# Optimization experiments

Measured on AMD Instinct MI355X. Metric: run time of the kernel, lower is better.

Reference implementation:

```python
import jax, jax.numpy as jnp
import numpy as np

N_NODES = 50000
N_EDGES = 500000
D_MODEL = 256
N_HEADS = 8
D_K = D_MODEL // N_HEADS


def setup_inputs() -> dict:
    key = jax.random.key(0)
    ks = jax.random.split(key, 12)
    s = 1.0 / np.sqrt(D_MODEL)
    inp = {
        "query": jax.random.normal(ks[0], (N_NODES, D_MODEL), dtype=jnp.float32),
        "key": jax.random.normal(ks[1], (N_NODES, D_MODEL), dtype=jnp.float32),
        "value": jax.random.normal(ks[2], (N_NODES, D_MODEL), dtype=jnp.float32),
        "edges": jax.random.randint(ks[3], (2, N_EDGES), 0, N_NODES, dtype=jnp.int64),
        # four nn.Linear(d_model, d_model) layers: q, k, v, out
        "Wq": jax.random.uniform(ks[4], (D_MODEL, D_MODEL), jnp.float32, -s, s),
        "bq": jax.random.uniform(ks[5], (D_MODEL,), jnp.float32, -s, s),
        "Wk": jax.random.uniform(ks[6], (D_MODEL, D_MODEL), jnp.float32, -s, s),
        "bk": jax.random.uniform(ks[7], (D_MODEL,), jnp.float32, -s, s),
        "Wv": jax.random.uniform(ks[8], (D_MODEL, D_MODEL), jnp.float32, -s, s),
        "bv": jax.random.uniform(ks[9], (D_MODEL,), jnp.float32, -s, s),
        "Wo": jax.random.uniform(ks[10], (D_MODEL, D_MODEL), jnp.float32, -s, s),
        "bo": jax.random.uniform(ks[11], (D_MODEL,), jnp.float32, -s, s),
    }
    return inp


def reference(query, key, value, edges, Wq, bq, Wk, bk, Wv, bv, Wo, bo):
    N = query.shape[0]
    # linear projections (torch Linear: x @ W.T + b), view as [N, h, d_k]
    q = (query @ Wq.T + bq).reshape(N, N_HEADS, D_K)
    k = (key @ Wk.T + bk).reshape(N, N_HEADS, D_K)
    v = (value @ Wv.T + bv).reshape(N, N_HEADS, D_K)

    dst, src = edges[0], edges[1]
    # per-edge dot-product scores [E, h]
    scores = jnp.einsum("ehd,ehd->eh", q[dst], k[src]) / jnp.sqrt(
        jnp.asarray(D_K, dtype=q.dtype)
    )
    # segment softmax over destination node neighborhoods (per head)
    m = jax.ops.segment_max(scores, dst, num_segments=N)  # [N, h]
    ex = jnp.exp(scores - m[dst])
    den = jax.ops.segment_sum(ex, dst, num_segments=N)  # [N, h]
    p_attn = ex / den[dst]  # [E, h]

    # weighted scatter-sum of gathered values -> [N, h, d_k]
    out = jax.ops.segment_sum(p_attn[:, :, None] * v[src], dst, num_segments=N)
    out = out.reshape(N, D_MODEL)
    return out @ Wo.T + bo
```

## Files before the change

### kernel.cpp

```cpp
#include <hip/hip_runtime.h>
#include <hip/hip_bf16.h>
#include <cstdint>

#define D_MODEL 256
#define NHEADS 8
#define DK 32
#define LDSPAD 4
#define LDSROW (D_MODEL + LDSPAD)
#define BM 64

typedef float f32x4 __attribute__((ext_vector_type(4)));
typedef __bf16 bf16x8 __attribute__((ext_vector_type(8)));

__device__ __forceinline__ unsigned short f2bf_rne(float f) {
    unsigned int u = __float_as_uint(f);
    u += 0x7FFF + ((u >> 16) & 1);
    return (unsigned short)(u >> 16);
}
__device__ __forceinline__ float bf2f(unsigned short h) {
    return __uint_as_float(((unsigned int)h) << 16);
}

__global__ void conv_weights_hist(const float* __restrict__ W0, const float* __restrict__ W1,
                                  const float* __restrict__ W2, const float* __restrict__ W3,
                                  unsigned short* __restrict__ out,
                                  const int* __restrict__ dst, int E,
                                  int* __restrict__ counts) {
    int i = blockIdx.x * blockDim.x + threadIdx.x;
    if (i < 4 * 8192) {
        const int w    = i >> 13;
        const int rem  = i & 8191;
        const int lane = rem & 63;
        const int kk   = (rem >> 6) & 7;
        const int ntile= rem >> 9;
        const int row  = ntile * 16 + (lane & 15);
        const int col  = kk * 32 + (lane >> 4) * 8;
        const float* Wsrc = (w == 0) ? W0 : (w == 1) ? W1 : (w == 2) ? W2 : W3;
        const float* sp = Wsrc + (size_t)row * D_MODEL + col;
        float4 x0 = *(const float4*)sp;
        float4 x1 = *(const float4*)(sp + 4);
        unsigned short* dp = out + (size_t)w * D_MODEL * D_MODEL + (size_t)rem * 8;
        ushort4 o0, o1;
        o0.x = f2bf_rne(x0.x); o0.y = f2bf_rne(x0.y); o0.z = f2bf_rne(x0.z); o0.w = f2bf_rne(x0.w);
        o1.x = f2bf_rne(x1.x); o1.y = f2bf_rne(x1.y); o1.z = f2bf_rne(x1.z); o1.w = f2bf_rne(x1.w);
        *(ushort4*)dp = o0;
        *(ushort4*)(dp + 4) = o1;
    } else {
        const int e = i - 4 * 8192;
        if (e < E) atomicAdd(&counts[dst[e]], 1);
    }
}

__global__ __launch_bounds__(512, 4) void gemm_qkv(
    const float* __restrict__ Aq, const float* __restrict__ Ak, const float* __restrict__ Av,
    const unsigned short* __restrict__ Wsw,
    const float* __restrict__ bq, const float* __restrict__ bk, const float* __restrict__ bv,
    unsigned short* __restrict__ qbuf, unsigned short* __restrict__ kvbuf,
    int M)
{
    __shared__ __align__(16) unsigned short smem[BM * LDSROW];

    const int which = blockIdx.y;
    const float* A = (which == 0) ? Aq : (which == 1) ? Ak : Av;
    const float* bias = (which == 0) ? bq : (which == 1) ? bk : bv;
    const unsigned short* Wb = Wsw + (size_t)which * D_MODEL * D_MODEL;
    unsigned short* outp = (which == 0) ? qbuf : kvbuf;
    const int out_stride = (which == 0) ? D_MODEL : 2 * D_MODEL;
    const int out_off    = (which == 2) ? D_MODEL : 0;

    const int lane  = threadIdx.x & 63;
    const int wave  = threadIdx.x >> 6;
    const int mrow  = lane & 15;
    const int quad  = lane >> 4;
    const int m0    = blockIdx.x * BM;

    bf16x8 bfr[2][8];
#pragma unroll
    for (int ni = 0; ni < 2; ++ni)
#pragma unroll
        for (int kk = 0; kk < 8; ++kk)
            bfr[ni][kk] = *(const bf16x8*)(Wb + ((size_t)((wave * 2 + ni) * 8 + kk) * 64 + lane) * 8);

    float bcol[2];
#pragma unroll
    for (int ni = 0; ni < 2; ++ni) bcol[ni] = bias[wave * 32 + ni * 16 + mrow];

#pragma unroll
    for (int half = 0; half < 2; ++half) {
        float4 x[4];
#pragma unroll
        for (int i = 0; i < 4; ++i) {
            const int g = (half * 4 + i) * 512 + threadIdx.x;
            const int r = g >> 6, c4 = g & 63;
            const int grow = min(m0 + r, M - 1);
            x[i] = *(const float4*)(A + (size_t)grow * D_MODEL + c4 * 4);
        }
#pragma unroll
        for (int i = 0; i < 4; ++i) {
            const int g = (half * 4 + i) * 512 + threadIdx.x;
            const int r = g >> 6, c4 = g & 63;
            ushort4 o;
            o.x = f2bf_rne(x[i].x); o.y = f2bf_rne(x[i].y);
            o.z = f2bf_rne(x[i].z); o.w = f2bf_rne(x[i].w);
            *(ushort4*)(smem + r * LDSROW + c4 * 4) = o;
        }
    }
    __syncthreads();

    f32x4 acc[4][2] = {};
#pragma unroll
    for (int kk = 0; kk < 8; ++kk) {
        bf16x8 afr[4];
#pragma unroll
        for (int mi = 0; mi < 4; ++mi)
            afr[mi] = *(const bf16x8*)(smem + (mi * 16 + mrow) * LDSROW + kk * 32 + quad * 8);
#pragma unroll
        for (int mi = 0; mi < 4; ++mi)
#pragma unroll
            for (int ni = 0; ni < 2; ++ni)
                acc[mi][ni] = __builtin_amdgcn_mfma_f32_16x16x32_bf16(
                    afr[mi], bfr[ni][kk], acc[mi][ni], 0, 0, 0);
    }

#pragma unroll
    for (int mi = 0; mi < 4; ++mi)
#pragma unroll
        for (int r = 0; r < 4; ++r) {
            const int row = m0 + mi * 16 + quad * 4 + r;
            if (row < M) {
#pragma unroll
                for (int ni = 0; ni < 2; ++ni)
                    outp[(size_t)row * out_stride + out_off + wave * 32 + ni * 16 + mrow] =
                        f2bf_rne(acc[mi][ni][r] + bcol[ni]);
            }
        }
}

__global__ __launch_bounds__(512, 4) void gemm_out(
    const unsigned short* __restrict__ Ab, const unsigned short* __restrict__ Wb,
    const float* __restrict__ bias, float* __restrict__ outp, int M)
{
    __shared__ __align__(16) unsigned short smem[BM * LDSROW];

    const int lane  = threadIdx.x & 63;
    const int wave  = threadIdx.x >> 6;
    const int mrow  = lane & 15;
    const int quad  = lane >> 4;
    const int m0    = blockIdx.x * BM;

    bf16x8 bfr[2][8];
#pragma unroll
    for (int ni = 0; ni < 2; ++ni)
#pragma unroll
        for (int kk = 0; kk < 8; ++kk)
            bfr[ni][kk] = *(const bf16x8*)(Wb + ((size_t)((wave * 2 + ni) * 8 + kk) * 64 + lane) * 8);

    float bcol[2];
#pragma unroll
    for (int ni = 0; ni < 2; ++ni) bcol[ni] = bias[wave * 32 + ni * 16 + mrow];

#pragma unroll
    for (int i = 0; i < 4; ++i) {
        const int g = i * 512 + threadIdx.x;
        const int r = g >> 5, c8 = g & 31;
        const int grow = min(m0 + r, M - 1);
        bf16x8 x = *(const bf16x8*)(Ab + (size_t)grow * D_MODEL + c8 * 8);
        *(bf16x8*)(smem + r * LDSROW + c8 * 8) = x;
    }
    __syncthreads();

    f32x4 acc[4][2] = {};
#pragma unroll
    for (int kk = 0; kk < 8; ++kk) {
        bf16x8 afr[4];
#pragma unroll
        for (int mi = 0; mi < 4; ++mi)
            afr[mi] = *(const bf16x8*)(smem + (mi * 16 + mrow) * LDSROW + kk * 32 + quad * 8);
#pragma unroll
        for (int mi = 0; mi < 4; ++mi)
#pragma unroll
            for (int ni = 0; ni < 2; ++ni)
                acc[mi][ni] = __builtin_amdgcn_mfma_f32_16x16x32_bf16(
                    afr[mi], bfr[ni][kk], acc[mi][ni], 0, 0, 0);
    }

#pragma unroll
    for (int mi = 0; mi < 4; ++mi)
#pragma unroll
        for (int r = 0; r < 4; ++r) {
            const int row = m0 + mi * 16 + quad * 4 + r;
            if (row < M) {
#pragma unroll
                for (int ni = 0; ni < 2; ++ni)
                    outp[(size_t)row * D_MODEL + wave * 32 + ni * 16 + mrow] =
                        acc[mi][ni][r] + bcol[ni];
            }
        }
}

__global__ void block_reduce_kernel(const int* __restrict__ counts, int N,
                                    int* __restrict__ blockSums) {
    const int g = blockIdx.x * 256 + threadIdx.x;
    int v = (g < N) ? counts[g] : 0;
#pragma unroll
    for (int d = 1; d < 64; d <<= 1) v += __shfl_xor(v, d);
    __shared__ int ws[4];
    if ((threadIdx.x & 63) == 0) ws[threadIdx.x >> 6] = v;
    __syncthreads();
    if (threadIdx.x == 0) blockSums[blockIdx.x] = ws[0] + ws[1] + ws[2] + ws[3];
}

__global__ void scan_blocks_kernel(int* __restrict__ blockSums, int G) {
    __shared__ int sh[256];
    const int t = threadIdx.x;
    int v = (t < G) ? blockSums[t] : 0;
    sh[t] = v;
    __syncthreads();
#pragma unroll
    for (int off = 1; off < 256; off <<= 1) {
        int add = (t >= off) ? sh[t - off] : 0;
        __syncthreads();
        sh[t] += add;
        __syncthreads();
    }
    if (t < G) blockSums[t] = sh[t] - v;
}

__global__ void scan_write_kernel(const int* __restrict__ counts, int N,
                                  const int* __restrict__ blockOffsets,
                                  int* __restrict__ offsets) {
    const int g = blockIdx.x * 256 + threadIdx.x;
    const int t = threadIdx.x;
    int v = (g < N) ? counts[g] : 0;
    __shared__ int sh[256];
    sh[t] = v;
    __syncthreads();
#pragma unroll
    for (int off = 1; off < 256; off <<= 1) {
        int add = (t >= off) ? sh[t - off] : 0;
        __syncthreads();
        sh[t] += add;
        __syncthreads();
    }
    if (g <= N) offsets[g] = sh[t] - v + blockOffsets[blockIdx.x];
}

__global__ void fill_kernel(const int* __restrict__ dst, const int* __restrict__ src, int E,
                            const int* __restrict__ offsets, int* __restrict__ cursor,
                            int* __restrict__ ssrc) {
    int i = blockIdx.x * blockDim.x + threadIdx.x;
    if (i < E) {
        int d = dst[i];
        int r = atomicAdd(&cursor[d], 1);
        ssrc[offsets[d] + r] = src[i];
    }
}

__global__ __launch_bounds__(256) void attn_kernel(
    const unsigned short* __restrict__ qb, const unsigned short* __restrict__ kv,
    const int* __restrict__ offsets, const int* __restrict__ ssrc,
    unsigned short* __restrict__ attn, int N)
{
    const int node = blockIdx.x * 4 + (threadIdx.x >> 6);
    if (node >= N) return;
    const int lane = threadIdx.x & 63;

    ushort4 qu = *(const ushort4*)(qb + (size_t)node * D_MODEL + 4 * lane);
    const float sc = 0.17677669529663689f;
    float qx = bf2f(qu.x) * sc, qy = bf2f(qu.y) * sc,
          qz = bf2f(qu.z) * sc, qw = bf2f(qu.w) * sc;

    float m = -INFINITY, l = 0.f;
    float ax = 0.f, ay = 0.f, az = 0.f, aw = 0.f;

    const int e0 = offsets[node], e1 = offsets[node + 1];
    int e = e0;

    for (; e + 7 < e1; e += 8) {
        const unsigned short* b0 = kv + (size_t)ssrc[e]     * 512 + 4 * lane;
        const unsigned short* b1 = kv + (size_t)ssrc[e + 1] * 512 + 4 * lane;
        const unsigned short* b2 = kv + (size_t)ssrc[e + 2] * 512 + 4 * lane;
        const unsigned short* b3 = kv + (size_t)ssrc[e + 3] * 512 + 4 * lane;
        const unsigned short* b4 = kv + (size_t)ssrc[e + 4] * 512 + 4 * lane;
        const unsigned short* b5 = kv + (size_t)ssrc[e + 5] * 512 + 4 * lane;
        const unsigned short* b6 = kv + (size_t)ssrc[e + 6] * 512 + 4 * lane;
        const unsigned short* b7 = kv + (size_t)ssrc[e + 7] * 512 + 4 * lane;
        ushort4 k0 = *(const ushort4*)b0, v0 = *(const ushort4*)(b0 + D_MODEL);
        ushort4 k1 = *(const ushort4*)b1, v1 = *(const ushort4*)(b1 + D_MODEL);
        ushort4 k2 = *(const ushort4*)b2, v2 = *(const ushort4*)(b2 + D_MODEL);
        ushort4 k3 = *(const ushort4*)b3, v3 = *(const ushort4*)(b3 + D_MODEL);
        ushort4 k4 = *(const ushort4*)b4, v4 = *(const ushort4*)(b4 + D_MODEL);
        ushort4 k5 = *(const ushort4*)b5, v5 = *(const ushort4*)(b5 + D_MODEL);
        ushort4 k6 = *(const ushort4*)b6, v6 = *(const ushort4*)(b6 + D_MODEL);
        ushort4 k7 = *(const ushort4*)b7, v7 = *(const ushort4*)(b7 + D_MODEL);

        float p0 = qx * bf2f(k0.x) + qy * bf2f(k0.y) + qz * bf2f(k0.z) + qw * bf2f(k0.w);
        float p1 = qx * bf2f(k1.x) + qy * bf2f(k1.y) + qz * bf2f(k1.z) + qw * bf2f(k1.w);
        float p2 = qx * bf2f(k2.x) + qy * bf2f(k2.y) + qz * bf2f(k2.z) + qw * bf2f(k2.w);
        float p3 = qx * bf2f(k3.x) + qy * bf2f(k3.y) + qz * bf2f(k3.z) + qw * bf2f(k3.w);
        float p4 = qx * bf2f(k4.x) + qy * bf2f(k4.y) + qz * bf2f(k4.z) + qw * bf2f(k4.w);
        float p5 = qx * bf2f(k5.x) + qy * bf2f(k5.y) + qz * bf2f(k5.z) + qw * bf2f(k5.w);
        float p6 = qx * bf2f(k6.x) + qy * bf2f(k6.y) + qz * bf2f(k6.z) + qw * bf2f(k6.w);
        float p7 = qx * bf2f(k7.x) + qy * bf2f(k7.y) + qz * bf2f(k7.z) + qw * bf2f(k7.w);
#pragma unroll
        for (int d = 1; d <= 4; d <<= 1) {
            p0 += __shfl_xor(p0, d); p1 += __shfl_xor(p1, d);
            p2 += __shfl_xor(p2, d); p3 += __shfl_xor(p3, d);
            p4 += __shfl_xor(p4, d); p5 += __shfl_xor(p5, d);
            p6 += __shfl_xor(p6, d); p7 += __shfl_xor(p7, d);
        }
        float mnew = fmaxf(fmaxf(fmaxf(fmaxf(m, p0), fmaxf(p1, p2)), fmaxf(fmaxf(p3, p4), fmaxf(p5, p6))), p7);
        float alpha = __expf(m - mnew);
        float w0 = __expf(p0 - mnew), w1 = __expf(p1 - mnew);
        float w2 = __expf(p2 - mnew), w3 = __expf(p3 - mnew);
        float w4 = __expf(p4 - mnew), w5 = __expf(p5 - mnew);
        float w6 = __expf(p6 - mnew), w7 = __expf(p7 - mnew);
        ax = ax * alpha + w0 * bf2f(v0.x) + w1 * bf2f(v1.x) + w2 * bf2f(v2.x) + w3 * bf2f(v3.x)
                        + w4 * bf2f(v4.x) + w5 * bf2f(v5.x) + w6 * bf2f(v6.x) + w7 * bf2f(v7.x);
        ay = ay * alpha + w0 * bf2f(v0.y) + w1 * bf2f(v1.y) + w2 * bf2f(v2.y) + w3 * bf2f(v3.y)
                        + w4 * bf2f(v4.y) + w5 * bf2f(v5.y) + w6 * bf2f(v6.y) + w7 * bf2f(v7.y);
        az = az * alpha + w0 * bf2f(v0.z) + w1 * bf2f(v1.z) + w2 * bf2f(v2.z) + w3 * bf2f(v3.z)
                        + w4 * bf2f(v4.z) + w5 * bf2f(v5.z) + w6 * bf2f(v6.z) + w7 * bf2f(v7.z);
        aw = aw * alpha + w0 * bf2f(v0.w) + w1 * bf2f(v1.w) + w2 * bf2f(v2.w) + w3 * bf2f(v3.w)
                        + w4 * bf2f(v4.w) + w5 * bf2f(v5.w) + w6 * bf2f(v6.w) + w7 * bf2f(v7.w);
        l = l * alpha + w0 + w1 + w2 + w3 + w4 + w5 + w6 + w7;
        m = mnew;
    }

    for (; e + 3 < e1; e += 4) {
        const unsigned short* b0 = kv + (size_t)ssrc[e]     * 512 + 4 * lane;
        const unsigned short* b1 = kv + (size_t)ssrc[e + 1] * 512 + 4 * lane;
        const unsigned short* b2 = kv + (size_t)ssrc[e + 2] * 512 + 4 * lane;
        const unsigned short* b3 = kv + (size_t)ssrc[e + 3] * 512 + 4 * lane;
        ushort4 k0 = *(const ushort4*)b0, v0 = *(const ushort4*)(b0 + D_MODEL);
        ushort4 k1 = *(const ushort4*)b1, v1 = *(const ushort4*)(b1 + D_MODEL);
        ushort4 k2 = *(const ushort4*)b2, v2 = *(const ushort4*)(b2 + D_MODEL);
        ushort4 k3 = *(const ushort4*)b3, v3 = *(const ushort4*)(b3 + D_MODEL);

        float p0 = qx * bf2f(k0.x) + qy * bf2f(k0.y) + qz * bf2f(k0.z) + qw * bf2f(k0.w);
        float p1 = qx * bf2f(k1.x) + qy * bf2f(k1.y) + qz * bf2f(k1.z) + qw * bf2f(k1.w);
        float p2 = qx * bf2f(k2.x) + qy * bf2f(k2.y) + qz * bf2f(k2.z) + qw * bf2f(k2.w);
        float p3 = qx * bf2f(k3.x) + qy * bf2f(k3.y) + qz * bf2f(k3.z) + qw * bf2f(k3.w);
#pragma unroll
        for (int d = 1; d <= 4; d <<= 1) {
            p0 += __shfl_xor(p0, d); p1 += __shfl_xor(p1, d);
            p2 += __shfl_xor(p2, d); p3 += __shfl_xor(p3, d);
        }
        float mnew = fmaxf(fmaxf(fmaxf(m, p0), fmaxf(p1, p2)), p3);
        float alpha = __expf(m - mnew);
        float w0 = __expf(p0 - mnew), w1 = __expf(p1 - mnew);
        float w2 = __expf(p2 - mnew), w3 = __expf(p3 - mnew);
        ax = ax * alpha + w0 * bf2f(v0.x) + w1 * bf2f(v1.x) + w2 * bf2f(v2.x) + w3 * bf2f(v3.x);
        ay = ay * alpha + w0 * bf2f(v0.y) + w1 * bf2f(v1.y) + w2 * bf2f(v2.y) + w3 * bf2f(v3.y);
        az = az * alpha + w0 * bf2f(v0.z) + w1 * bf2f(v1.z) + w2 * bf2f(v2.z) + w3 * bf2f(v3.z);
        aw = aw * alpha + w0 * bf2f(v0.w) + w1 * bf2f(v1.w) + w2 * bf2f(v2.w) + w3 * bf2f(v3.w);
        l = l * alpha + w0 + w1 + w2 + w3;
        m = mnew;
    }

    for (; e < e1; ++e) {
        const unsigned short* b = kv + (size_t)ssrc[e] * 512 + 4 * lane;
        ushort4 ku = *(const ushort4*)b;
        ushort4 vu = *(const ushort4*)(b + D_MODEL);
        float p = qx * bf2f(ku.x) + qy * bf2f(ku.y) + qz * bf2f(ku.z) + qw * bf2f(ku.w);
        p += __shfl_xor(p, 1);
        p += __shfl_xor(p, 2);
        p += __shfl_xor(p, 4);
        float mnew  = fmaxf(m, p);
        float alpha = __expf(m - mnew);
        float w     = __expf(p - mnew);
        ax = ax * alpha + w * bf2f(vu.x);
        ay = ay * alpha + w * bf2f(vu.y);
        az = az * alpha + w * bf2f(vu.z);
        aw = aw * alpha + w * bf2f(vu.w);
        l = l * alpha + w;
        m = mnew;
    }

    const float inv = (l > 0.f) ? 1.f / l : 0.f;
    ushort4 o;
    o.x = f2bf_rne(ax * inv);
    o.y = f2bf_rne(ay * inv);
    o.z = f2bf_rne(az * inv);
    o.w = f2bf_rne(aw * inv);
    *(ushort4*)(attn + (size_t)node * D_MODEL + 4 * lane) = o;
}

extern "C" void kernel_launch(void* const* d_in, const int* in_sizes, int n_in,
                              void* d_out, int out_size, void* d_ws, size_t ws_size,
                              hipStream_t stream)
{
    const float* query = (const float*)d_in[0];
    const float* key   = (const float*)d_in[1];
    const float* value = (const float*)d_in[2];
    const int*   edges = (const int*)d_in[3];
    const float* Wq = (const float*)d_in[4];
    const float* bq = (const float*)d_in[5];
    const float* Wk = (const float*)d_in[6];
    const float* bk = (const float*)d_in[7];
    const float* Wv = (const float*)d_in[8];
    const float* bv = (const float*)d_in[9];
    const float* Wo = (const float*)d_in[10];
    const float* bo = (const float*)d_in[11];
    float* out = (float*)d_out;

    const int N = in_sizes[0] / D_MODEL;
    const int E = in_sizes[3] / 2;
    const int* dst = edges;
    const int* src = edges + E;

    char* ws = (char*)d_ws;
    size_t off = 0;
    auto alloc = [&](size_t bytes) {
        void* p = ws + off;
        off += (bytes + 255) & ~(size_t)255;
        return p;
    };
    unsigned short* qbuf  = (unsigned short*)alloc((size_t)N * D_MODEL * 2);
    unsigned short* kvbuf = (unsigned short*)alloc((size_t)N * 2 * D_MODEL * 2);
    unsigned short* attnb = (unsigned short*)alloc((size_t)N * D_MODEL * 2);
    unsigned short* Wbuf  = (unsigned short*)alloc((size_t)4 * D_MODEL * D_MODEL * 2);
    int*            counts  = (int*)alloc((size_t)2 * N * 4);
    int*            offsets = (int*)alloc((size_t)(N + 1) * 4);
    int*            ssrc    = (int*)alloc((size_t)E * 4);
    int*            bsums   = (int*)alloc((size_t)256 * 4);

    hipMemsetAsync(counts, 0, (size_t)2 * N * 4, stream);

    const int fused_threads = 4 * 8192 + E;
    conv_weights_hist<<<(fused_threads + 255) / 256, 256, 0, stream>>>(
        Wq, Wk, Wv, Wo, Wbuf, dst, E, counts);

    const int mtiles = (N + BM - 1) / BM;
    gemm_qkv<<<dim3(mtiles, 3), 512, 0, stream>>>(query, key, value, Wbuf,
                                                  bq, bk, bv, qbuf, kvbuf, N);

    const int G = (N + 256) / 256;
    block_reduce_kernel<<<G, 256, 0, stream>>>(counts, N, bsums);
    scan_blocks_kernel<<<1, 256, 0, stream>>>(bsums, G);
    scan_write_kernel<<<G, 256, 0, stream>>>(counts, N, bsums, offsets);

    const int eblocks = (E + 255) / 256;
    fill_kernel<<<eblocks, 256, 0, stream>>>(dst, src, E, offsets, counts + N, ssrc);
    attn_kernel<<<(N + 3) / 4, 256, 0, stream>>>(qbuf, kvbuf, offsets, ssrc, attnb, N);

    gemm_out<<<mtiles, 512, 0, stream>>>(attnb, Wbuf + 3 * D_MODEL * D_MODEL, bo, out, N);
}
```

Before: 371.5 us.

## Make projection GEMMs persistent with register-prefetched double-buffered LDS tiles

```diff
diff --git a/kernel.cpp b/kernel.cpp
--- a/kernel.cpp
+++ b/kernel.cpp
@@ -7,7 +7,9 @@
 #define DK 32
 #define LDSPAD 4
 #define LDSROW (D_MODEL + LDSPAD)
-#define BM 64
+#define QBM 32
+#define QBLK 171
+#define OBLK 512
 
 typedef float f32x4 __attribute__((ext_vector_type(4)));
 typedef __bf16 bf16x8 __attribute__((ext_vector_type(8)));
@@ -56,9 +58,9 @@
     const unsigned short* __restrict__ Wsw,
     const float* __restrict__ bq, const float* __restrict__ bk, const float* __restrict__ bv,
     unsigned short* __restrict__ qbuf, unsigned short* __restrict__ kvbuf,
-    int M)
+    int M, int mtiles)
 {
-    __shared__ __align__(16) unsigned short smem[BM * LDSROW];
+    __shared__ __align__(16) unsigned short smem[2 * QBM * LDSROW];
 
     const int which = blockIdx.y;
     const float* A = (which == 0) ? Aq : (which == 1) ? Ak : Av;
@@ -72,7 +74,6 @@
     const int wave  = threadIdx.x >> 6;
     const int mrow  = lane & 15;
     const int quad  = lane >> 4;
-    const int m0    = blockIdx.x * BM;
 
     bf16x8 bfr[2][8];
 #pragma unroll
@@ -85,68 +86,94 @@
 #pragma unroll
     for (int ni = 0; ni < 2; ++ni) bcol[ni] = bias[wave * 32 + ni * 16 + mrow];
 
-#pragma unroll
-    for (int half = 0; half < 2; ++half) {
-        float4 x[4];
+    int t = blockIdx.x;
+    float4 pf[4];
+    if (t < mtiles) {
+        const int m0 = t * QBM;
 #pragma unroll
         for (int i = 0; i < 4; ++i) {
-            const int g = (half * 4 + i) * 512 + threadIdx.x;
+            const int g = i * 512 + threadIdx.x;
             const int r = g >> 6, c4 = g & 63;
             const int grow = min(m0 + r, M - 1);
-            x[i] = *(const float4*)(A + (size_t)grow * D_MODEL + c4 * 4);
-        }
+            pf[i] = *(const float4*)(A + (size_t)grow * D_MODEL + c4 * 4);
+        }
+    }
+
+    int cur = 0;
+    for (; t < mtiles; t += QBLK) {
+        const int m0 = t * QBM;
+        unsigned short* buf = smem + cur * (QBM * LDSROW);
+
 #pragma unroll
         for (int i = 0; i < 4; ++i) {
-            const int g = (half * 4 + i) * 512 + threadIdx.x;
+            const int g = i * 512 + threadIdx.x;
             const int r = g >> 6, c4 = g & 63;
             ushort4 o;
-            o.x = f2bf_rne(x[i].x); o.y = f2bf_rne(x[i].y);
-            o.z = f2bf_rne(x[i].z); o.w = f2bf_rne(x[i].w);
-            *(ushort4*)(smem + r * LDSROW + c4 * 4) = o;
-        }
-    }
-    __syncthreads();
-
-    f32x4 acc[4][2] = {};
-#pragma unroll
-    for (int kk = 0; kk < 8; ++kk) {
-        bf16x8 afr[4];
-#pragma unroll
-        for (int mi = 0; mi < 4; ++mi)
-            afr[mi] = *(const bf16x8*)(smem + (mi * 16 + mrow) * LDSROW + kk * 32 + quad * 8);
-#pragma unroll
-        for (int mi = 0; mi < 4; ++mi)
-#pragma unroll
-            for (int ni = 0; ni < 2; ++ni)
-                acc[mi][ni] = __builtin_amdgcn_mfma_f32_16x16x32_bf16(
-                    afr[mi], bfr[ni][kk], acc[mi][ni], 0, 0, 0);
-    }
-
-#pragma unroll
-    for (int mi = 0; mi < 4; ++mi)
-#pragma unroll
-        for (int r = 0; r < 4; ++r) {
-            const int row = m0 + mi * 16 + quad * 4 + r;
-            if (row < M) {
+            o.x = f2bf_rne(pf[i].x); o.y = f2bf_rne(pf[i].y);
+            o.z = f2bf_rne(pf[i].z); o.w = f2bf_rne(pf[i].w);
+            *(ushort4*)(buf + r * LDSROW + c4 * 4) = o;
+        }
+
+        const int tn = t + QBLK;
+        if (tn < mtiles) {
+            const int m0n = tn * QBM;
+#pragma unroll
+            for (int i = 0; i < 4; ++i) {
+                const int g = i * 512 + threadIdx.x;
+                const int r = g >> 6, c4 = g & 63;
+                const int grow = min(m0n + r, M - 1);
+                pf[i] = *(const float4*)(A + (size_t)grow * D_MODEL + c4 * 4);
+            }
+        }
+
+        asm volatile("s_waitcnt lgkmcnt(0)" ::: "memory");
+        __builtin_amdgcn_s_barrier();
+        __builtin_amdgcn_sched_barrier(0);
+
+        f32x4 acc[2][2] = {};
+#pragma unroll
+        for (int kk = 0; kk < 8; ++kk) {
+            bf16x8 afr[2];
+#pragma unroll
+            for (int mi = 0; mi < 2; ++mi)
+                afr[mi] = *(const bf16x8*)(buf + (mi * 16 + mrow) * LDSROW + kk * 32 + quad * 8);
+#pragma unroll
+            for (int mi = 0; mi < 2; ++mi)
 #pragma unroll
                 for (int ni = 0; ni < 2; ++ni)
-                    outp[(size_t)row * out_stride + out_off + wave * 32 + ni * 16 + mrow] =
-                        f2bf_rne(acc[mi][ni][r] + bcol[ni]);
+                    acc[mi][ni] = __builtin_amdgcn_mfma_f32_16x16x32_bf16(
+                        afr[mi], bfr[ni][kk], acc[mi][ni], 0, 0, 0);
+        }
+
+#pragma unroll
+        for (int mi = 0; mi < 2; ++mi)
+#pragma unroll
+            for (int r = 0; r < 4; ++r) {
+                const int row = m0 + mi * 16 + quad * 4 + r;
+                if (row < M) {
+#pragma unroll
+                    for (int ni = 0; ni < 2; ++ni)
+                        outp[(size_t)row * out_stride + out_off + wave * 32 + ni * 16 + mrow] =
+                            f2bf_rne(acc[mi][ni][r] + bcol[ni]);
+                }
             }
-        }
+
+        __builtin_amdgcn_s_barrier();
+        __builtin_amdgcn_sched_barrier(0);
+        cur ^= 1;
+    }
 }
 
 __global__ __launch_bounds__(512, 4) void gemm_out(
     const unsigned short* __restrict__ Ab, const unsigned short* __restrict__ Wb,
-    const float* __restrict__ bias, float* __restrict__ outp, int M)
+    const float* __restrict__ bias, float* __restrict__ outp, int M, int mtiles)
 {
-    __shared__ __align__(16) unsigned short smem[BM * LDSROW];
+    __shared__ __align__(16) unsigned short smem[2 * QBM * LDSROW];
 
     const int lane  = threadIdx.x & 63;
     const int wave  = threadIdx.x >> 6;
     const int mrow  = lane & 15;
     const int quad  = lane >> 4;
-    const int m0    = blockIdx.x * BM;
 
     bf16x8 bfr[2][8];
 #pragma unroll
@@ -159,43 +186,79 @@
 #pragma unroll
     for (int ni = 0; ni < 2; ++ni) bcol[ni] = bias[wave * 32 + ni * 16 + mrow];
 
-#pragma unroll
-    for (int i = 0; i < 4; ++i) {
-        const int g = i * 512 + threadIdx.x;
-        const int r = g >> 5, c8 = g & 31;
-        const int grow = min(m0 + r, M - 1);
-        bf16x8 x = *(const bf16x8*)(Ab + (size_t)grow * D_MODEL + c8 * 8);
-        *(bf16x8*)(smem + r * LDSROW + c8 * 8) = x;
-    }
-    __syncthreads();
-
-    f32x4 acc[4][2] = {};
-#pragma unroll
-    for (int kk = 0; kk < 8; ++kk) {
-        bf16x8 afr[4];
-#pragma unroll
-        for (int mi = 0; mi < 4; ++mi)
-            afr[mi] = *(const bf16x8*)(smem + (mi * 16 + mrow) * LDSROW + kk * 32 + quad * 8);
-#pragma unroll
-        for (int mi = 0; mi < 4; ++mi)
-#pragma unroll
-            for (int ni = 0; ni < 2; ++ni)
-                acc[mi][ni] = __builtin_amdgcn_mfma_f32_16x16x32_bf16(
-                    afr[mi], bfr[ni][kk], acc[mi][ni], 0, 0, 0);
-    }
-
-#pragma unroll
-    for (int mi = 0; mi < 4; ++mi)
-#pragma unroll
-        for (int r = 0; r < 4; ++r) {
-            const int row = m0 + mi * 16 + quad * 4 + r;
-            if (row < M) {
+    int t = blockIdx.x;
+    bf16x8 pf[2];
+    if (t < mtiles) {
+        const int m0 = t * QBM;
+#pragma unroll
+        for (int i = 0; i < 2; ++i) {
+            const int g = i * 512 + threadIdx.x;
+            const int r = g >> 5, c8 = g & 31;
+            const int grow = min(m0 + r, M - 1);
+            pf[i] = *(const bf16x8*)(Ab + (size_t)grow * D_MODEL + c8 * 8);
+        }
+    }
+
+    int cur = 0;
+    for (; t < mtiles; t += OBLK) {
+        const int m0 = t * QBM;
+        unsigned short* buf = smem + cur * (QBM * LDSROW);
+
+#pragma unroll
+        for (int i = 0; i < 2; ++i) {
+            const int g = i * 512 + threadIdx.x;
+            const int r = g >> 5, c8 = g & 31;
+            *(bf16x8*)(buf + r * LDSROW + c8 * 8) = pf[i];
+        }
+
+        const int tn = t + OBLK;
+        if (tn < mtiles) {
+            const int m0n = tn * QBM;
+#pragma unroll
+            for (int i = 0; i < 2; ++i) {
+                const int g = i * 512 + threadIdx.x;
+                const int r = g >> 5, c8 = g & 31;
+                const int grow = min(m0n + r, M - 1);
+                pf[i] = *(const bf16x8*)(Ab + (size_t)grow * D_MODEL + c8 * 8);
+            }
+        }
+
+        asm volatile("s_waitcnt lgkmcnt(0)" ::: "memory");
+        __builtin_amdgcn_s_barrier();
+        __builtin_amdgcn_sched_barrier(0);
+
+        f32x4 acc[2][2] = {};
+#pragma unroll
+        for (int kk = 0; kk < 8; ++kk) {
+            bf16x8 afr[2];
+#pragma unroll
+            for (int mi = 0; mi < 2; ++mi)
+                afr[mi] = *(const bf16x8*)(buf + (mi * 16 + mrow) * LDSROW + kk * 32 + quad * 8);
+#pragma unroll
+            for (int mi = 0; mi < 2; ++mi)
 #pragma unroll
                 for (int ni = 0; ni < 2; ++ni)
-                    outp[(size_t)row * D_MODEL + wave * 32 + ni * 16 + mrow] =
-                        acc[mi][ni][r] + bcol[ni];
+                    acc[mi][ni] = __builtin_amdgcn_mfma_f32_16x16x32_bf16(
+                        afr[mi], bfr[ni][kk], acc[mi][ni], 0, 0, 0);
+        }
+
+#pragma unroll
+        for (int mi = 0; mi < 2; ++mi)
+#pragma unroll
+            for (int r = 0; r < 4; ++r) {
+                const int row = m0 + mi * 16 + quad * 4 + r;
+                if (row < M) {
+#pragma unroll
+                    for (int ni = 0; ni < 2; ++ni)
+                        outp[(size_t)row * D_MODEL + wave * 32 + ni * 16 + mrow] =
+                            acc[mi][ni][r] + bcol[ni];
+                }
             }
-        }
+
+        __builtin_amdgcn_s_barrier();
+        __builtin_amdgcn_sched_barrier(0);
+        cur ^= 1;
+    }
 }
 
 __global__ void block_reduce_kernel(const int* __restrict__ counts, int N,
@@ -431,9 +494,9 @@
     conv_weights_hist<<<(fused_threads + 255) / 256, 256, 0, stream>>>(
         Wq, Wk, Wv, Wo, Wbuf, dst, E, counts);
 
-    const int mtiles = (N + BM - 1) / BM;
-    gemm_qkv<<<dim3(mtiles, 3), 512, 0, stream>>>(query, key, value, Wbuf,
-                                                  bq, bk, bv, qbuf, kvbuf, N);
+    const int mtiles = (N + QBM - 1) / QBM;
+    gemm_qkv<<<dim3(QBLK, 3), 512, 0, stream>>>(query, key, value, Wbuf,
+                                                bq, bk, bv, qbuf, kvbuf, N, mtiles);
 
     const int G = (N + 256) / 256;
     block_reduce_kernel<<<G, 256, 0, stream>>>(counts, N, bsums);
@@ -444,5 +507,5 @@
     fill_kernel<<<eblocks, 256, 0, stream>>>(dst, src, E, offsets, counts + N, ssrc);
     attn_kernel<<<(N + 3) / 4, 256, 0, stream>>>(qbuf, kvbuf, offsets, ssrc, attnb, N);
 
-    gemm_out<<<mtiles, 512, 0, stream>>>(attnb, Wbuf + 3 * D_MODEL * D_MODEL, bo, out, N);
-}
+    gemm_out<<<OBLK, 512, 0, stream>>>(attnb, Wbuf + 3 * D_MODEL * D_MODEL, bo, out, N, mtiles);
+}
```

Result: slower. 415.3 us (+11.8%).
